# Optimization experiments

Measured on AMD Instinct MI355X. Metric: run time of the kernel, lower is better.

Reference implementation:

```python
import jax, jax.numpy as jnp
import numpy as np

N_NODES = 10000
N_EDGES = 320000
N_GRAPHS = 64
L = 3  # num_layers


def _gru(a, h, wih, whh, bih, bhh):
    # torch.nn.GRUCell math: input a, hidden h
    gi = a @ wih.T + bih
    gh = h @ whh.T + bhh
    ir, iz, inn = jnp.split(gi, 3, axis=-1)
    hr, hz, hn = jnp.split(gh, 3, axis=-1)
    r = jax.nn.sigmoid(ir + hr)
    z = jax.nn.sigmoid(iz + hz)
    n = jnp.tanh(inn + r * hn)
    return (1.0 - z) * n + z * h


def _ggc(x, src, dst, w, wih, whh, bih, bhh):
    # PyG GatedGraphConv: pad features up to out_channels, then L rounds of
    # (linear -> scatter-add over edges -> GRUCell update)
    out_ch = w.shape[-1]
    if x.shape[-1] < out_ch:
        x = jnp.concatenate(
            [x, jnp.zeros((x.shape[0], out_ch - x.shape[-1]), x.dtype)], axis=-1)
    for i in range(w.shape[0]):
        m = x @ w[i]                                        # [N, C]
        a = jax.ops.segment_sum(m[src], dst, num_segments=N_NODES)  # scatter-add
        x = _gru(a, x, wih, whh, bih, bhh)
    return x


def setup_inputs() -> dict:
    key = jax.random.key(0)
    ks = jax.random.split(key, 16)
    d1, d2 = 128, 256
    s1, s2 = 1.0 / np.sqrt(d1), 1.0 / np.sqrt(d2)
    x = jax.random.normal(ks[0], (N_NODES, d1), dtype=jnp.float32)
    edge_index = jax.random.randint(ks[1], (2, N_EDGES), 0, N_NODES, dtype=jnp.int64)
    batch = jnp.sort(jax.random.randint(ks[2], (N_NODES,), 0, N_GRAPHS, dtype=jnp.int64))
    return {
        "x": x,
        "edge_index": edge_index,
        "batch": batch,
        "w1": jax.random.normal(ks[3], (L, d1, d1), jnp.float32) * s1,
        "gru1_wih": jax.random.normal(ks[4], (3 * d1, d1), jnp.float32) * s1,
        "gru1_whh": jax.random.normal(ks[5], (3 * d1, d1), jnp.float32) * s1,
        "gru1_bih": jax.random.normal(ks[6], (3 * d1,), jnp.float32) * s1,
        "gru1_bhh": jax.random.normal(ks[7], (3 * d1,), jnp.float32) * s1,
        "w2": jax.random.normal(ks[8], (L, d2, d2), jnp.float32) * s2,
        "gru2_wih": jax.random.normal(ks[9], (3 * d2, d2), jnp.float32) * s2,
        "gru2_whh": jax.random.normal(ks[10], (3 * d2, d2), jnp.float32) * s2,
        "gru2_bih": jax.random.normal(ks[11], (3 * d2,), jnp.float32) * s2,
        "gru2_bhh": jax.random.normal(ks[12], (3 * d2,), jnp.float32) * s2,
        "fc_w": jax.random.normal(ks[13], (6, d2), jnp.float32) * s2,
        "fc_b": jnp.zeros((6,), jnp.float32),
    }


def reference(x, edge_index, batch, w1, gru1_wih, gru1_whh, gru1_bih, gru1_bhh,
              w2, gru2_wih, gru2_whh, gru2_bih, gru2_bhh, fc_w, fc_b):
    src, dst = edge_index[0], edge_index[1]
    y = jax.nn.relu(_ggc(x, src, dst, w1, gru1_wih, gru1_whh, gru1_bih, gru1_bhh))
    y = _ggc(y, src, dst, w2, gru2_wih, gru2_whh, gru2_bih, gru2_bhh)
    y = jax.ops.segment_max(y, batch, num_segments=N_GRAPHS)  # global max pool [G, 256]
    return y @ fc_w.T + fc_b  # [G, 6]
```

## Files before the change

kernel.cpp:

```cpp
#include <hip/hip_runtime.h>

#define NN 10000
#define NNP 10112
#define NE 320000
#define NG 64
#define D1 128
#define D2 256
#define MT 158

typedef unsigned short u16;
typedef short v8s __attribute__((ext_vector_type(8)));
typedef float v4f __attribute__((ext_vector_type(4)));

__device__ __forceinline__ u16 f2bf(float x) {
    unsigned u = __float_as_uint(x);
    return (u16)((u + 0x7fffu + ((u >> 16) & 1u)) >> 16);
}
__device__ __forceinline__ float bf2f(u16 b) {
    return __uint_as_float(((unsigned)b) << 16);
}
__device__ __forceinline__ float sigm(float x) { return 1.f / (1.f + __expf(-x)); }
__device__ __forceinline__ float tanh_f(float x) {
    float cx = fminf(fmaxf(x, -15.f), 15.f);
    float e = __expf(2.f * cx);
    return (e - 1.f) / (e + 1.f);
}

#define MF(d, a, b) d = __builtin_amdgcn_mfma_f32_16x16x32_bf16(a, b, d, 0, 0, 0)

#define GLDS16(gp, lp)                                                         \
    __builtin_amdgcn_global_load_lds(                                          \
        (__attribute__((address_space(1))) unsigned int*)(unsigned long long)(gp), \
        (__attribute__((address_space(3))) unsigned int*)(lp), 16, 0, 0)

#define SWZ(bx, by)                              \
    const int bid_ = blockIdx.x;                 \
    const int l_ = bid_ >> 3;                    \
    const int by = (bid_ & 7) * 20 + l_ % 20;    \
    const int bx = l_ / 20;                      \
    if (by >= MT) return;


__global__ __launch_bounds__(256)
void mm_k(const u16* __restrict__ Ah, const u16* __restrict__ Al,
          const u16* __restrict__ Bh, const u16* __restrict__ Bl,
          float* __restrict__ Cm, int K) {
    SWZ(bx, by)
    __shared__ u16 lds[16384];
    const int tid = threadIdx.x;
    const int wave = tid >> 6, lane = tid & 63;
    const int wm = (wave >> 1) * 32, wn = (wave & 1) * 32;
    const int bm = by * 64, bn = bx * 64;
    const int quad = lane >> 4, r16 = lane & 15;
    const int NK = K >> 5;
    const size_t arow = (size_t)(bm >> 6) * (K >> 3);
    const size_t brow = (size_t)(bn >> 6) * (K >> 3);

    auto STAGE = [&](int b, int k0) {
        const u16* pa_h = Ah + (arow + (k0 >> 3)) * 512;
        const u16* pa_l = Al + (arow + (k0 >> 3)) * 512;
        const u16* pb_h = Bh + (brow + (k0 >> 3)) * 512;
        const u16* pb_l = Bl + (brow + (k0 >> 3)) * 512;
        const int B = b * 8192;
#pragma unroll
        for (int t = 0; t < 4; ++t) {
            int u = (t << 2) | wave;
            const u16* gp; int ld;
            if (u < 4)       { gp = pa_h + u * 512;        ld = B + u * 512; }
            else if (u < 8)  { gp = pa_l + (u - 4) * 512;  ld = B + 2048 + (u - 4) * 512; }
            else if (u < 12) { gp = pb_h + (u - 8) * 512;  ld = B + 4096 + (u - 8) * 512; }
            else             { gp = pb_l + (u - 12) * 512; ld = B + 6144 + (u - 12) * 512; }
            GLDS16(gp + lane * 8, &lds[ld]);
        }
    };

    v4f acc[2][2] = {};
    STAGE(0, 0);
    __syncthreads();
    int cur = 0;
    for (int ks = 0; ks < NK; ++ks) {
        if (ks + 1 < NK) STAGE(cur ^ 1, (ks + 1) << 5);
        const int B = cur * 8192;
        v8s af[2], alf[2], bf[2], blf[2];
#pragma unroll
        for (int i = 0; i < 2; ++i) {
            int ra = B + quad * 512 + (wm + i * 16 + r16) * 8;
            int rb = B + quad * 512 + (wn + i * 16 + r16) * 8;
            af[i]  = *(const v8s*)&lds[ra];
            alf[i] = *(const v8s*)&lds[2048 + ra];
            bf[i]  = *(const v8s*)&lds[4096 + rb];
            blf[i] = *(const v8s*)&lds[6144 + rb];
        }
#pragma unroll
        for (int i = 0; i < 2; ++i)
#pragma unroll
            for (int j = 0; j < 2; ++j) {
                MF(acc[i][j], af[i], bf[j]);
                MF(acc[i][j], af[i], blf[j]);
                MF(acc[i][j], alf[i], bf[j]);
            }
        __syncthreads();
        cur ^= 1;
    }
#pragma unroll
    for (int i = 0; i < 2; ++i) {
        int gr0 = bm + wm + i * 16 + quad * 4;
#pragma unroll
        for (int j = 0; j < 2; ++j) {
            int gc = bn + wn + j * 16 + r16;
#pragma unroll
            for (int r = 0; r < 4; ++r) {
                int gr = gr0 + r;
                if (gr < NN) Cm[(size_t)gr * K + gc] = acc[i][j][r];
            }
        }
    }
}

template<int MODE, int OS>
__global__ __launch_bounds__(256)
void giqru_k(const u16* __restrict__ Ah, const u16* __restrict__ Al,
             const u16* __restrict__ Xh, const u16* __restrict__ Xl,
             const u16* __restrict__ WcH, const u16* __restrict__ WcL,
             const float* __restrict__ bih, const float* __restrict__ bhh,
             u16* __restrict__ xh_out, u16* __restrict__ xl_out,
             const int* __restrict__ batch, unsigned* __restrict__ pool,
             int C) {
    SWZ(bx, by)
    __shared__ u16 lds[24576];
    const int tid = threadIdx.x;
    const int wave = tid >> 6, lane = tid & 63;
    const int wm = (wave >> 1) * 32, wn = (wave & 1) * 64;
    const int bm = by * 64, bn = bx * 128;
    const int quad = lane >> 4, r16 = lane & 15;
    const int K2 = 2 * C;
    const int NK = K2 >> 5;
    const int CCH = C >> 3;
    const size_t arow = (size_t)(bm >> 6) * CCH;
    const size_t wrow = (size_t)(bn >> 7) * (K2 >> 3);

    auto STAGE = [&](int b, int k0) {
        const u16* sh; const u16* sl; int kk;
        if (k0 < C) { sh = Ah; sl = Al; kk = k0; } else { sh = Xh; sl = Xl; kk = k0 - C; }
        const u16* pa_h = sh + (arow + (kk >> 3)) * 512;
        const u16* pa_l = sl + (arow + (kk >> 3)) * 512;
        const u16* pw_h = WcH + (wrow + (k0 >> 3)) * 1024;
        const u16* pw_l = WcL + (wrow + (k0 >> 3)) * 1024;
        const int B = b * 12288;
#pragma unroll
        for (int t = 0; t < 6; ++t) {
            int u = (t << 2) | wave;
            const u16* gp; int ld;
            if (u < 4)       { gp = pa_h + u * 512;        ld = B + u * 512; }
            else if (u < 8)  { gp = pa_l + (u - 4) * 512;  ld = B + 2048 + (u - 4) * 512; }
            else if (u < 16) { gp = pw_h + (u - 8) * 512;  ld = B + 4096 + (u - 8) * 512; }
            else             { gp = pw_l + (u - 16) * 512; ld = B + 8192 + (u - 16) * 512; }
            GLDS16(gp + lane * 8, &lds[ld]);
        }
    };

    v4f acc[2][4] = {};
    STAGE(0, 0);
    __syncthreads();
    int cur = 0;
    for (int ks = 0; ks < NK; ++ks) {
        const int k0 = ks << 5;
        if (ks + 1 < NK) STAGE(cur ^ 1, (ks + 1) << 5);
        const int B = cur * 12288;
        const bool ap = (k0 < C);
        const int g2 = ap ? 2 : 3;
        v8s w0h, w0l, w1h, w1l, w2h, w2l;
        {
            int p0 = B + 4096 + quad * 1024 + (wn + r16) * 8;
            w0h = *(const v8s*)&lds[p0];
            w0l = *(const v8s*)&lds[4096 + p0];
            w1h = *(const v8s*)&lds[p0 + 128];
            w1l = *(const v8s*)&lds[4096 + p0 + 128];
            w2h = *(const v8s*)&lds[p0 + g2 * 128];
            w2l = *(const v8s*)&lds[4096 + p0 + g2 * 128];
        }
#pragma unroll
        for (int i = 0; i < 2; ++i) {
            int ra = B + quad * 512 + (wm + i * 16 + r16) * 8;
            v8s fah = *(const v8s*)&lds[ra];
            v8s fal = *(const v8s*)&lds[2048 + ra];
            MF(acc[i][0], fah, w0h); MF(acc[i][0], fah, w0l); MF(acc[i][0], fal, w0h);
            MF(acc[i][1], fah, w1h); MF(acc[i][1], fah, w1l); MF(acc[i][1], fal, w1h);
            if (ap) {
                MF(acc[i][2], fah, w2h); MF(acc[i][2], fah, w2l); MF(acc[i][2], fal, w2h);
            } else {
                MF(acc[i][3], fah, w2h); MF(acc[i][3], fah, w2l); MF(acc[i][3], fal, w2h);
            }
        }
        __syncthreads();
        cur ^= 1;
    }

    const int c = bx * 32 + (wn ? 16 : 0) + r16;
    const float br = bih[c] + bhh[c];
    const float bz = bih[C + c] + bhh[C + c];
    const float bi_n = bih[2 * C + c];
    const float bh_n = bhh[2 * C + c];
    const int cch = c >> 3, cr = c & 7;
#pragma unroll
    for (int i = 0; i < 2; ++i) {
        int R0 = bm + wm + i * 16 + quad * 4;
#pragma unroll
        for (int r = 0; r < 4; ++r) {
            int R = R0 + r;
            if (R >= NN) continue;
            float rr = sigm(acc[i][0][r] + br);
            float zz = sigm(acc[i][1][r] + bz);
            float nn_ = tanh_f(acc[i][2][r] + bi_n + rr * (acc[i][3][r] + bh_n));
            size_t hx = ((size_t)(R >> 6) * CCH + cch) * 512 + ((R & 63) << 3) + cr;
            float h = bf2f(Xh[hx]) + bf2f(Xl[hx]);
            float o = (1.f - zz) * nn_ + zz * h;
            if (MODE == 2) {
                unsigned b = __float_as_uint(o);
                unsigned u = (b & 0x80000000u) ? ~b : (b | 0x80000000u);
                atomicMax(&pool[batch[R] * 256 + c], u);
            } else {
                if (MODE == 1) o = fmaxf(o, 0.f);
                size_t ox = ((size_t)(R >> 6) * (OS >> 3) + cch) * 512 + ((R & 63) << 3) + cr;
                u16 hh = f2bf(o);
                xh_out[ox] = hh;
                xl_out[ox] = f2bf(o - bf2f(hh));
            }
        }
    }
}

__global__ void count_k(const int* __restrict__ dst, int* __restrict__ cnt) {
    int e = blockIdx.x * blockDim.x + threadIdx.x;
    if (e < NE) atomicAdd(&cnt[dst[e]], 1);
}

__global__ void scan_k(const int* __restrict__ cnt, int* __restrict__ off,
                       int* __restrict__ cur) {
    __shared__ int ps[1024];
    const int tid = threadIdx.x;
    const int CH = (NN + 1023) / 1024;
    const int base = tid * CH;
    int s = 0;
    for (int i = 0; i < CH; ++i) {
        int idx = base + i;
        if (idx < NN) s += cnt[idx];
    }
    ps[tid] = s;
    __syncthreads();
    for (int d = 1; d < 1024; d <<= 1) {
        int v = (tid >= d) ? ps[tid - d] : 0;
        __syncthreads();
        ps[tid] += v;
        __syncthreads();
    }
    int run = (tid > 0) ? ps[tid - 1] : 0;
    for (int i = 0; i < CH; ++i) {
        int idx = base + i;
        if (idx <= NN) { off[idx] = run; if (idx < NN) cur[idx] = run; }
        if (idx < NN) run += cnt[idx];
    }
}

__global__ void fill_k(const int* __restrict__ src, const int* __restrict__ dst,
                       int* __restrict__ cur, int* __restrict__ elist) {
    int e = blockIdx.x * blockDim.x + threadIdx.x;
    if (e >= NE) return;
    int p = atomicAdd(&cur[dst[e]], 1);
    elist[p] = src[e];
}

template<int C>
__global__ void gather_k(const float* __restrict__ m, const int* __restrict__ off,
                         const int* __restrict__ elist,
                         u16* __restrict__ ah, u16* __restrict__ al) {
    constexpr int LPN = C / 4;
    int t = blockIdx.x * blockDim.x + threadIdx.x;
    int node = t / LPN;
    if (node >= NN) return;
    int c = (t % LPN) * 4;
    int s0 = off[node], s1 = off[node + 1];
    v4f a0 = 0.f, a1 = 0.f, a2 = 0.f, a3 = 0.f;
    int i = s0;
    for (; i + 4 <= s1; i += 4) {
        int e0 = elist[i], e1 = elist[i + 1], e2 = elist[i + 2], e3 = elist[i + 3];
        v4f v0 = *(const v4f*)(m + (size_t)e0 * C + c);
        v4f v1 = *(const v4f*)(m + (size_t)e1 * C + c);
        v4f v2 = *(const v4f*)(m + (size_t)e2 * C + c);
        v4f v3 = *(const v4f*)(m + (size_t)e3 * C + c);
        a0 += v0; a1 += v1; a2 += v2; a3 += v3;
    }
    for (; i < s1; ++i) {
        int e = elist[i];
        a0 += *(const v4f*)(m + (size_t)e * C + c);
    }
    v4f acc = (a0 + a1) + (a2 + a3);
    ushort4 h, l;
    h.x = f2bf(acc[0]); l.x = f2bf(acc[0] - bf2f(h.x));
    h.y = f2bf(acc[1]); l.y = f2bf(acc[1] - bf2f(h.y));
    h.z = f2bf(acc[2]); l.z = f2bf(acc[2] - bf2f(h.z));
    h.w = f2bf(acc[3]); l.w = f2bf(acc[3] - bf2f(h.w));
    size_t ox = ((size_t)(node >> 6) * (C >> 3) + (c >> 3)) * 512 + ((node & 63) << 3) + (c & 7);
    *(ushort4*)(ah + ox) = h;
    *(ushort4*)(al + ox) = l;
}

__global__ void prep_k(const float* __restrict__ w1, const float* __restrict__ w2,
                       const float* __restrict__ wih1, const float* __restrict__ whh1,
                       const float* __restrict__ wih2, const float* __restrict__ whh2,
                       const float* __restrict__ xin,
                       u16* __restrict__ B1h, u16* __restrict__ B1l,
                       u16* __restrict__ B2h, u16* __restrict__ B2l,
                       u16* __restrict__ Wc1h, u16* __restrict__ Wc1l,
                       u16* __restrict__ Wc2h, u16* __restrict__ Wc2l,
                       u16* __restrict__ xh, u16* __restrict__ xl) {
    const int n1 = 3 * D1 * D1;
    const int n2 = 3 * D2 * D2;
    const int c1 = 4 * D1 * 2 * D1;
    const int c2 = 4 * D2 * 2 * D2;
    int t = blockIdx.x * blockDim.x + threadIdx.x;
    if (t < n1) {
        int l = t / (D1 * D1), rem = t - l * (D1 * D1);
        int k = rem / D1, n = rem - k * D1;
        float v = w1[t]; u16 h = f2bf(v);
        size_t o = l * D1 * D1 + ((size_t)(n >> 6) * (D1 >> 3) + (k >> 3)) * 512 + ((n & 63) << 3) + (k & 7);
        B1h[o] = h; B1l[o] = f2bf(v - bf2f(h)); return;
    }
    t -= n1;
    if (t < n2) {
        int l = t / (D2 * D2), rem = t - l * (D2 * D2);
        int k = rem / D2, n = rem - k * D2;
        float v = w2[t]; u16 h = f2bf(v);
        size_t o = l * D2 * D2 + ((size_t)(n >> 6) * (D2 >> 3) + (k >> 3)) * 512 + ((n & 63) << 3) + (k & 7);
        B2h[o] = h; B2l[o] = f2bf(v - bf2f(h)); return;
    }
    t -= n2;
    if (t < c1) {
        int jp = t >> 8, k = t & 255;
        int c = ((jp >> 6) << 4) | (jp & 15);
        int g = (jp >> 4) & 3;
        float v;
        if (g == 0)      v = (k < D1) ? wih1[c * D1 + k]            : whh1[c * D1 + k - D1];
        else if (g == 1) v = (k < D1) ? wih1[(D1 + c) * D1 + k]     : whh1[(D1 + c) * D1 + k - D1];
        else if (g == 2) v = (k < D1) ? wih1[(2 * D1 + c) * D1 + k] : 0.f;
        else             v = (k < D1) ? 0.f : whh1[(2 * D1 + c) * D1 + k - D1];
        u16 h = f2bf(v);
        size_t o = ((size_t)(jp >> 7) * 32 + (k >> 3)) * 1024 + ((jp & 127) << 3) + (k & 7);
        Wc1h[o] = h; Wc1l[o] = f2bf(v - bf2f(h)); return;
    }
    t -= c1;
    if (t < c2) {
        int jp = t >> 9, k = t & 511;
        int c = ((jp >> 6) << 4) | (jp & 15);
        int g = (jp >> 4) & 3;
        float v;
        if (g == 0)      v = (k < D2) ? wih2[c * D2 + k]            : whh2[c * D2 + k - D2];
        else if (g == 1) v = (k < D2) ? wih2[(D2 + c) * D2 + k]     : whh2[(D2 + c) * D2 + k - D2];
        else if (g == 2) v = (k < D2) ? wih2[(2 * D2 + c) * D2 + k] : 0.f;
        else             v = (k < D2) ? 0.f : whh2[(2 * D2 + c) * D2 + k - D2];
        u16 h = f2bf(v);
        size_t o = ((size_t)(jp >> 7) * 64 + (k >> 3)) * 1024 + ((jp & 127) << 3) + (k & 7);
        Wc2h[o] = h; Wc2l[o] = f2bf(v - bf2f(h)); return;
    }
    t -= c2;
    if (t < NN * D1) {
        int n = t >> 7, cc = t & 127;
        float v = xin[t];
        u16 h = f2bf(v);
        size_t o = ((size_t)(n >> 6) * 16 + (cc >> 3)) * 512 + ((n & 63) << 3) + (cc & 7);
        xh[o] = h;
        xl[o] = f2bf(v - bf2f(h));
    }
}

__global__ void pad_k(u16* __restrict__ xh, u16* __restrict__ xl) {
    int t = blockIdx.x * blockDim.x + threadIdx.x;
    if (t >= NNP * 128) return;
    int n = t >> 7, c = 128 + (t & 127);
    size_t o = ((size_t)(n >> 6) * 32 + (c >> 3)) * 512 + ((n & 63) << 3) + (c & 7);
    xh[o] = 0;
    xl[o] = 0;
}

__global__ void pool_init_k(unsigned* __restrict__ pool) {
    int t = blockIdx.x * blockDim.x + threadIdx.x;
    if (t < NG * D2) pool[t] = 0x007FFFFFu;
}

__global__ void fc_k(const unsigned* __restrict__ pool, const float* __restrict__ w,
                     const float* __restrict__ b, float* __restrict__ out) {
    int t = blockIdx.x * blockDim.x + threadIdx.x;
    if (t >= NG * 6) return;
    int g = t / 6, o = t - g * 6;
    float s = b[o];
    for (int c = 0; c < D2; ++c) {
        unsigned u = pool[g * D2 + c];
        unsigned bits = (u & 0x80000000u) ? (u ^ 0x80000000u) : ~u;
        s += __uint_as_float(bits) * w[o * D2 + c];
    }
    out[t] = s;
}

extern "C" void kernel_launch(void* const* d_in, const int* in_sizes, int n_in,
                              void* d_out, int out_size, void* d_ws, size_t ws_size,
                              hipStream_t stream) {
    const float* x_in = (const float*)d_in[0];
    const int* ei = (const int*)d_in[1];
    const int* src = ei;
    const int* dst = ei + NE;
    const int* batch = (const int*)d_in[2];
    const float* w1   = (const float*)d_in[3];
    const float* wih1 = (const float*)d_in[4];
    const float* whh1 = (const float*)d_in[5];
    const float* bih1 = (const float*)d_in[6];
    const float* bhh1 = (const float*)d_in[7];
    const float* w2   = (const float*)d_in[8];
    const float* wih2 = (const float*)d_in[9];
    const float* whh2 = (const float*)d_in[10];
    const float* bih2 = (const float*)d_in[11];
    const float* bhh2 = (const float*)d_in[12];
    const float* fcw  = (const float*)d_in[13];
    const float* fcb  = (const float*)d_in[14];
    float* out = (float*)d_out;

    float* ws = (float*)d_ws;
    float* mbuf = ws;
    u16* a_h  = (u16*)(mbuf + (size_t)NNP * 256);
    u16* a_l  = a_h + (size_t)NNP * 256;
    u16* xA0h = a_l + (size_t)NNP * 256;
    u16* xA0l = xA0h + (size_t)NNP * 128;
    u16* xA1h = xA0l + (size_t)NNP * 128;
    u16* xA1l = xA1h + (size_t)NNP * 128;
    u16* xB0h = xA1l + (size_t)NNP * 128;
    u16* xB0l = xB0h + (size_t)NNP * 256;
    u16* xB1h = xB0l + (size_t)NNP * 256;
    u16* xB1l = xB1h + (size_t)NNP * 256;
    u16* B1h  = xB1l + (size_t)NNP * 256;
    u16* B1l  = B1h + 3 * D1 * D1;
    u16* B2h  = B1l + 3 * D1 * D1;
    u16* B2l  = B2h + 3 * D2 * D2;
    u16* Wc1h = B2l + 3 * D2 * D2;
    u16* Wc1l = Wc1h + 4 * D1 * 2 * D1;
    u16* Wc2h = Wc1l + 4 * D1 * 2 * D1;
    u16* Wc2l = Wc2h + 4 * D2 * 2 * D2;
    int* cnt   = (int*)(Wc2l + 4 * D2 * 2 * D2);
    int* off   = cnt + NN;
    int* cur   = off + NN + 1;
    int* elist = cur + NN;
    unsigned* pool = (unsigned*)(elist + NE);

    hipMemsetAsync(cnt, 0, NN * sizeof(int), stream);
    count_k<<<(NE + 255) / 256, 256, 0, stream>>>(dst, cnt);
    scan_k<<<1, 1024, 0, stream>>>(cnt, off, cur);
    fill_k<<<(NE + 255) / 256, 256, 0, stream>>>(src, dst, cur, elist);
    {
        int total = 3 * D1 * D1 + 3 * D2 * D2 + 4 * D1 * 2 * D1 + 4 * D2 * 2 * D2 + NN * D1;
        prep_k<<<(total + 255) / 256, 256, 0, stream>>>(
            w1, w2, wih1, whh1, wih2, whh2, x_in,
            B1h, B1l, B2h, B2l, Wc1h, Wc1l, Wc2h, Wc2l, xA0h, xA0l);
    }
    pad_k<<<(NNP * 128 + 255) / 256, 256, 0, stream>>>(xB0h, xB0l);
    pool_init_k<<<(NG * D2 + 255) / 256, 256, 0, stream>>>(pool);

    const int M1 = 160 * (D1 / 64);
    const int M2 = 160 * (D2 / 64);
    const int G1 = 160 * (D1 / 32);
    const int G2 = 160 * (D2 / 32);
    const int GG1 = (NN * (D1 / 4) + 255) / 256;
    const int GG2 = (NN * (D2 / 4) + 255) / 256;

    mm_k<<<M1, 256, 0, stream>>>(xA0h, xA0l, B1h, B1l, mbuf, D1);
    gather_k<D1><<<GG1, 256, 0, stream>>>(mbuf, off, elist, a_h, a_l);
    giqru_k<0, 128><<<G1, 256, 0, stream>>>(
        a_h, a_l, xA0h, xA0l, Wc1h, Wc1l, bih1, bhh1,
        xA1h, xA1l, nullptr, nullptr, D1);

    mm_k<<<M1, 256, 0, stream>>>(xA1h, xA1l, B1h + D1 * D1, B1l + D1 * D1, mbuf, D1);
    gather_k<D1><<<GG1, 256, 0, stream>>>(mbuf, off, elist, a_h, a_l);
    giqru_k<0, 128><<<G1, 256, 0, stream>>>(
        a_h, a_l, xA1h, xA1l, Wc1h, Wc1l, bih1, bhh1,
        xA0h, xA0l, nullptr, nullptr, D1);

    mm_k<<<M1, 256, 0, stream>>>(xA0h, xA0l, B1h + 2 * D1 * D1, B1l + 2 * D1 * D1, mbuf, D1);
    gather_k<D1><<<GG1, 256, 0, stream>>>(mbuf, off, elist, a_h, a_l);
    giqru_k<1, 256><<<G1, 256, 0, stream>>>(
        a_h, a_l, xA0h, xA0l, Wc1h, Wc1l, bih1, bhh1,
        xB0h, xB0l, nullptr, nullptr, D1);

    mm_k<<<M2, 256, 0, stream>>>(xB0h, xB0l, B2h, B2l, mbuf, D2);
    gather_k<D2><<<GG2, 256, 0, stream>>>(mbuf, off, elist, a_h, a_l);
    giqru_k<0, 256><<<G2, 256, 0, stream>>>(
        a_h, a_l, xB0h, xB0l, Wc2h, Wc2l, bih2, bhh2,
        xB1h, xB1l, nullptr, nullptr, D2);

    mm_k<<<M2, 256, 0, stream>>>(xB1h, xB1l, B2h + D2 * D2, B2l + D2 * D2, mbuf, D2);
    gather_k<D2><<<GG2, 256, 0, stream>>>(mbuf, off, elist, a_h, a_l);
    giqru_k<0, 256><<<G2, 256, 0, stream>>>(
        a_h, a_l, xB1h, xB1l, Wc2h, Wc2l, bih2, bhh2,
        xB0h, xB0l, nullptr, nullptr, D2);

    mm_k<<<M2, 256, 0, stream>>>(xB0h, xB0l, B2h + 2 * D2 * D2, B2l + 2 * D2 * D2, mbuf, D2);
    gather_k<D2><<<GG2, 256, 0, stream>>>(mbuf, off, elist, a_h, a_l);
    giqru_k<2, 256><<<G2, 256, 0, stream>>>(
        a_h, a_l, xB0h, xB0l, Wc2h, Wc2l, bih2, bhh2,
        nullptr, nullptr, batch, pool, D2);

    fc_k<<<1, 512, 0, stream>>>(pool, fcw, fcb, out);
}
```

Before: 584.3 us.

## Load MFMA fragments directly from global into registers, drop LDS staging

Both GEMM kernels stop staging tiles in shared memory with global_load_lds plus barriers. Each wave now loads its pre-tiled bf16 hi/lo fragments straight from global memory into registers, double-buffered in software across k-steps. The goal is to remove LDS round trips and __syncthreads, at the cost of more redundant global/L2 traffic, since waves sharing a tile each fetch it. The gather kernel also remaps block IDs so that consecutive node ranges land on the same XCD for better L2 locality.

```diff
diff --git a/kernel.cpp b/kernel.cpp
--- a/kernel.cpp
+++ b/kernel.cpp
@@ -28,11 +28,6 @@
 
 #define MF(d, a, b) d = __builtin_amdgcn_mfma_f32_16x16x32_bf16(a, b, d, 0, 0, 0)
 
-#define GLDS16(gp, lp)                                                         \
-    __builtin_amdgcn_global_load_lds(                                          \
-        (__attribute__((address_space(1))) unsigned int*)(unsigned long long)(gp), \
-        (__attribute__((address_space(3))) unsigned int*)(lp), 16, 0, 0)
-
 #define SWZ(bx, by)                              \
     const int bid_ = blockIdx.x;                 \
     const int l_ = bid_ >> 3;                    \
@@ -46,7 +41,6 @@
           const u16* __restrict__ Bh, const u16* __restrict__ Bl,
           float* __restrict__ Cm, int K) {
     SWZ(bx, by)
-    __shared__ u16 lds[16384];
     const int tid = threadIdx.x;
     const int wave = tid >> 6, lane = tid & 63;
     const int wm = (wave >> 1) * 32, wn = (wave & 1) * 32;
@@ -55,42 +49,23 @@
     const int NK = K >> 5;
     const size_t arow = (size_t)(bm >> 6) * (K >> 3);
     const size_t brow = (size_t)(bn >> 6) * (K >> 3);
-
-    auto STAGE = [&](int b, int k0) {
-        const u16* pa_h = Ah + (arow + (k0 >> 3)) * 512;
-        const u16* pa_l = Al + (arow + (k0 >> 3)) * 512;
-        const u16* pb_h = Bh + (brow + (k0 >> 3)) * 512;
-        const u16* pb_l = Bl + (brow + (k0 >> 3)) * 512;
-        const int B = b * 8192;
-#pragma unroll
-        for (int t = 0; t < 4; ++t) {
-            int u = (t << 2) | wave;
-            const u16* gp; int ld;
-            if (u < 4)       { gp = pa_h + u * 512;        ld = B + u * 512; }
-            else if (u < 8)  { gp = pa_l + (u - 4) * 512;  ld = B + 2048 + (u - 4) * 512; }
-            else if (u < 12) { gp = pb_h + (u - 8) * 512;  ld = B + 4096 + (u - 8) * 512; }
-            else             { gp = pb_l + (u - 12) * 512; ld = B + 6144 + (u - 12) * 512; }
-            GLDS16(gp + lane * 8, &lds[ld]);
+    const int aoff0 = (wm + r16) * 8;
+    const int boff0 = (wn + r16) * 8;
+
+    auto LOAD = [&](int ks, v8s* af, v8s* alf, v8s* bf, v8s* blf) {
+        const size_t ach = (arow + (size_t)(ks << 2) + quad) * 512;
+        const size_t bch = (brow + (size_t)(ks << 2) + quad) * 512;
+#pragma unroll
+        for (int i = 0; i < 2; ++i) {
+            af[i]  = *(const v8s*)(Ah + ach + aoff0 + i * 128);
+            alf[i] = *(const v8s*)(Al + ach + aoff0 + i * 128);
+            bf[i]  = *(const v8s*)(Bh + bch + boff0 + i * 128);
+            blf[i] = *(const v8s*)(Bl + bch + boff0 + i * 128);
         }
     };
 
     v4f acc[2][2] = {};
-    STAGE(0, 0);
-    __syncthreads();
-    int cur = 0;
-    for (int ks = 0; ks < NK; ++ks) {
-        if (ks + 1 < NK) STAGE(cur ^ 1, (ks + 1) << 5);
-        const int B = cur * 8192;
-        v8s af[2], alf[2], bf[2], blf[2];
-#pragma unroll
-        for (int i = 0; i < 2; ++i) {
-            int ra = B + quad * 512 + (wm + i * 16 + r16) * 8;
-            int rb = B + quad * 512 + (wn + i * 16 + r16) * 8;
-            af[i]  = *(const v8s*)&lds[ra];
-            alf[i] = *(const v8s*)&lds[2048 + ra];
-            bf[i]  = *(const v8s*)&lds[4096 + rb];
-            blf[i] = *(const v8s*)&lds[6144 + rb];
-        }
+    auto STEP = [&](v8s* af, v8s* alf, v8s* bf, v8s* blf) {
 #pragma unroll
         for (int i = 0; i < 2; ++i)
 #pragma unroll
@@ -99,9 +74,18 @@
                 MF(acc[i][j], af[i], blf[j]);
                 MF(acc[i][j], alf[i], bf[j]);
             }
-        __syncthreads();
-        cur ^= 1;
-    }
+    };
+
+    v8s aA[2], lA[2], bA[2], cA[2];
+    v8s aB[2], lB[2], bB[2], cB[2];
+    LOAD(0, aA, lA, bA, cA);
+    for (int ks = 0; ks < NK; ks += 2) {
+        LOAD(ks + 1, aB, lB, bB, cB);
+        STEP(aA, lA, bA, cA);
+        if (ks + 2 < NK) LOAD(ks + 2, aA, lA, bA, cA);
+        STEP(aB, lB, bB, cB);
+    }
+
 #pragma unroll
     for (int i = 0; i < 2; ++i) {
         int gr0 = bm + wm + i * 16 + quad * 4;
@@ -127,7 +111,6 @@
              const int* __restrict__ batch, unsigned* __restrict__ pool,
              int C) {
     SWZ(bx, by)
-    __shared__ u16 lds[24576];
     const int tid = threadIdx.x;
     const int wave = tid >> 6, lane = tid & 63;
     const int wm = (wave >> 1) * 32, wn = (wave & 1) * 64;
@@ -138,62 +121,53 @@
     const int CCH = C >> 3;
     const size_t arow = (size_t)(bm >> 6) * CCH;
     const size_t wrow = (size_t)(bn >> 7) * (K2 >> 3);
-
-    auto STAGE = [&](int b, int k0) {
-        const u16* sh; const u16* sl; int kk;
-        if (k0 < C) { sh = Ah; sl = Al; kk = k0; } else { sh = Xh; sl = Xl; kk = k0 - C; }
-        const u16* pa_h = sh + (arow + (kk >> 3)) * 512;
-        const u16* pa_l = sl + (arow + (kk >> 3)) * 512;
-        const u16* pw_h = WcH + (wrow + (k0 >> 3)) * 1024;
-        const u16* pw_l = WcL + (wrow + (k0 >> 3)) * 1024;
-        const int B = b * 12288;
-#pragma unroll
-        for (int t = 0; t < 6; ++t) {
-            int u = (t << 2) | wave;
-            const u16* gp; int ld;
-            if (u < 4)       { gp = pa_h + u * 512;        ld = B + u * 512; }
-            else if (u < 8)  { gp = pa_l + (u - 4) * 512;  ld = B + 2048 + (u - 4) * 512; }
-            else if (u < 16) { gp = pw_h + (u - 8) * 512;  ld = B + 4096 + (u - 8) * 512; }
-            else             { gp = pw_l + (u - 16) * 512; ld = B + 8192 + (u - 16) * 512; }
-            GLDS16(gp + lane * 8, &lds[ld]);
+    const int aoff0 = (wm + r16) * 8;
+    const int woff0 = (wn + r16) * 8;
+
+    auto LOAD = [&](int ks, v8s* fah, v8s* fal, v8s* wh, v8s* wl) {
+        const int k0 = ks << 5;
+        const bool ap = k0 < C;
+        const u16* sh = ap ? Ah : Xh;
+        const u16* sl = ap ? Al : Xl;
+        const int kk = ap ? k0 : k0 - C;
+        const size_t ach = (arow + (kk >> 3) + quad) * 512;
+        const size_t wch = (wrow + (k0 >> 3) + quad) * 1024;
+        const int g2 = ap ? 2 : 3;
+#pragma unroll
+        for (int i = 0; i < 2; ++i) {
+            fah[i] = *(const v8s*)(sh + ach + aoff0 + i * 128);
+            fal[i] = *(const v8s*)(sl + ach + aoff0 + i * 128);
+        }
+        wh[0] = *(const v8s*)(WcH + wch + woff0);
+        wl[0] = *(const v8s*)(WcL + wch + woff0);
+        wh[1] = *(const v8s*)(WcH + wch + woff0 + 128);
+        wl[1] = *(const v8s*)(WcL + wch + woff0 + 128);
+        wh[2] = *(const v8s*)(WcH + wch + woff0 + g2 * 128);
+        wl[2] = *(const v8s*)(WcL + wch + woff0 + g2 * 128);
+    };
+
+    v4f acc[2][4] = {};
+    auto STEP = [&](v8s* fah, v8s* fal, v8s* wh, v8s* wl, bool ap) {
+#pragma unroll
+        for (int i = 0; i < 2; ++i) {
+            MF(acc[i][0], fah[i], wh[0]); MF(acc[i][0], fah[i], wl[0]); MF(acc[i][0], fal[i], wh[0]);
+            MF(acc[i][1], fah[i], wh[1]); MF(acc[i][1], fah[i], wl[1]); MF(acc[i][1], fal[i], wh[1]);
+            if (ap) {
+                MF(acc[i][2], fah[i], wh[2]); MF(acc[i][2], fah[i], wl[2]); MF(acc[i][2], fal[i], wh[2]);
+            } else {
+                MF(acc[i][3], fah[i], wh[2]); MF(acc[i][3], fah[i], wl[2]); MF(acc[i][3], fal[i], wh[2]);
+            }
         }
     };
 
-    v4f acc[2][4] = {};
-    STAGE(0, 0);
-    __syncthreads();
-    int cur = 0;
-    for (int ks = 0; ks < NK; ++ks) {
-        const int k0 = ks << 5;
-        if (ks + 1 < NK) STAGE(cur ^ 1, (ks + 1) << 5);
-        const int B = cur * 12288;
-        const bool ap = (k0 < C);
-        const int g2 = ap ? 2 : 3;
-        v8s w0h, w0l, w1h, w1l, w2h, w2l;
-        {
-            int p0 = B + 4096 + quad * 1024 + (wn + r16) * 8;
-            w0h = *(const v8s*)&lds[p0];
-            w0l = *(const v8s*)&lds[4096 + p0];
-            w1h = *(const v8s*)&lds[p0 + 128];
-            w1l = *(const v8s*)&lds[4096 + p0 + 128];
-            w2h = *(const v8s*)&lds[p0 + g2 * 128];
-            w2l = *(const v8s*)&lds[4096 + p0 + g2 * 128];
-        }
-#pragma unroll
-        for (int i = 0; i < 2; ++i) {
-            int ra = B + quad * 512 + (wm + i * 16 + r16) * 8;
-            v8s fah = *(const v8s*)&lds[ra];
-            v8s fal = *(const v8s*)&lds[2048 + ra];
-            MF(acc[i][0], fah, w0h); MF(acc[i][0], fah, w0l); MF(acc[i][0], fal, w0h);
-            MF(acc[i][1], fah, w1h); MF(acc[i][1], fah, w1l); MF(acc[i][1], fal, w1h);
-            if (ap) {
-                MF(acc[i][2], fah, w2h); MF(acc[i][2], fah, w2l); MF(acc[i][2], fal, w2h);
-            } else {
-                MF(acc[i][3], fah, w2h); MF(acc[i][3], fah, w2l); MF(acc[i][3], fal, w2h);
-            }
-        }
-        __syncthreads();
-        cur ^= 1;
+    v8s ahA[2], alA[2], whA[3], wlA[3];
+    v8s ahB[2], alB[2], whB[3], wlB[3];
+    LOAD(0, ahA, alA, whA, wlA);
+    for (int ks = 0; ks < NK; ks += 2) {
+        LOAD(ks + 1, ahB, alB, whB, wlB);
+        STEP(ahA, alA, whA, wlA, (ks << 5) < C);
+        if (ks + 2 < NK) LOAD(ks + 2, ahA, alA, whA, wlA);
+        STEP(ahB, alB, whB, wlB, ((ks + 1) << 5) < C);
     }
 
     const int c = bx * 32 + (wn ? 16 : 0) + r16;
@@ -275,7 +249,11 @@
                          const int* __restrict__ elist,
                          u16* __restrict__ ah, u16* __restrict__ al) {
     constexpr int LPN = C / 4;
-    int t = blockIdx.x * blockDim.x + threadIdx.x;
+    const int GB = gridDim.x;
+    const int q = GB >> 3, r = GB & 7;
+    const int xx = blockIdx.x & 7, oo = blockIdx.x >> 3;
+    const int wg = (xx < r ? xx * (q + 1) : r * (q + 1) + (xx - r) * q) + oo;
+    int t = wg * 256 + threadIdx.x;
     int node = t / LPN;
     if (node >= NN) return;
     int c = (t % LPN) * 4;
```

Measured after the change: 557.6 us. -4.6%, faster.
